# Optimization experiments

Measured on AMD Instinct MI355X. Metric: run time of the kernel, lower is better.

Reference implementation:

```python
import jax, jax.numpy as jnp
import numpy as np

N = 50000          # nodes
E = 800000         # edges (avg degree 16)
ROLE_DIM = 16
LAY_DIM = 16
G_IN = 96          # graph_in
H = 96             # hidden_channels (two layers of 96)
G_OUT = 96         # graph_out
HID = 256          # dense hidden_dim
NUM_ROLES = 120
MAX_LAYOUT = 1025


def _lin_params(k, out_d, in_d, bias=True):
    kw, kb = jax.random.split(k)
    s = 1.0 / np.sqrt(in_d)
    W = jax.random.uniform(kw, (out_d, in_d), jnp.float32, -s, s)
    if bias:
        b = jax.random.uniform(kb, (out_d,), jnp.float32, -s, s)
        return W, b
    return W


def setup_inputs() -> dict:
    key = jax.random.key(0)
    ks = jax.random.split(key, 16)
    x_layout = jax.random.randint(ks[0], (N, 4), 0, MAX_LAYOUT)
    x_role = jax.random.randint(ks[1], (N,), 0, NUM_ROLES)
    edge_index = jax.random.randint(ks[2], (2, E), 0, N)
    layout_emb = jax.random.normal(ks[3], (MAX_LAYOUT, LAY_DIM), jnp.float32)
    role_emb = jax.random.normal(ks[4], (NUM_ROLES, ROLE_DIM), jnp.float32)
    lin_W, lin_b = _lin_params(ks[5], G_IN, ROLE_DIM + 4 * LAY_DIM)
    c0_lW, c0_lb = _lin_params(ks[6], H, G_IN)
    c0_rW = _lin_params(ks[7], H, G_IN, bias=False)
    c1_lW, c1_lb = _lin_params(ks[8], H, H)
    c1_rW = _lin_params(ks[9], H, H, bias=False)
    c2_lW, c2_lb = _lin_params(ks[10], G_OUT, H)
    c2_rW = _lin_params(ks[11], G_OUT, H, bias=False)
    d0_W, d0_b = _lin_params(ks[12], HID, G_OUT)
    d1_W, d1_b = _lin_params(ks[13], HID, HID)
    d2_W, d2_b = _lin_params(ks[14], 1, HID)
    return dict(x_layout=x_layout, x_role=x_role, edge_index=edge_index,
                layout_emb=layout_emb, role_emb=role_emb,
                lin_W=lin_W, lin_b=lin_b,
                c0_lW=c0_lW, c0_lb=c0_lb, c0_rW=c0_rW,
                c1_lW=c1_lW, c1_lb=c1_lb, c1_rW=c1_rW,
                c2_lW=c2_lW, c2_lb=c2_lb, c2_rW=c2_rW,
                d0_W=d0_W, d0_b=d0_b, d1_W=d1_W, d1_b=d1_b,
                d2_W=d2_W, d2_b=d2_b)


def _sage(x, src, dst, lW, lb, rW):
    # SAGEConv (mean aggr): out = lin_l(mean_{j->i} x_j) + lin_r(x_i)
    msg = x[src]                                               # [E, D] gather
    ssum = jax.ops.segment_sum(msg, dst, num_segments=N)       # [N, D]
    cnt = jax.ops.segment_sum(jnp.ones((src.shape[0],), x.dtype), dst,
                              num_segments=N)                  # [N]
    agg = ssum / jnp.maximum(cnt, 1.0)[:, None]
    return agg @ lW.T + lb + x @ rW.T


def reference(x_layout, x_role, edge_index, layout_emb, role_emb,
              lin_W, lin_b,
              c0_lW, c0_lb, c0_rW,
              c1_lW, c1_lb, c1_rW,
              c2_lW, c2_lb, c2_rW,
              d0_W, d0_b, d1_W, d1_b, d2_W, d2_b):
    # embed + concat: [N, 4*16] layout embeds + [N, 16] role embed
    lay = layout_emb[x_layout].reshape(x_layout.shape[0], 4 * LAY_DIM)
    x = jnp.concatenate([lay, role_emb[x_role]], axis=1)       # [N, 80]
    x = x @ lin_W.T + lin_b                                    # [N, G_IN]
    # masked_select with x_role != -100: all indices valid here -> identity
    src, dst = edge_index[0], edge_index[1]
    x = jax.nn.relu(_sage(x, src, dst, c0_lW, c0_lb, c0_rW))
    x = jax.nn.relu(_sage(x, src, dst, c1_lW, c1_lb, c1_rW))
    x = jax.nn.relu(_sage(x, src, dst, c2_lW, c2_lb, c2_rW))
    # dense head (dropout p=0 -> identity)
    x = jax.nn.relu(x @ d0_W.T + d0_b)
    x = jax.nn.relu(x @ d1_W.T + d1_b)
    return x @ d2_W.T + d2_b                                   # [N, 1]
```

## Files before the change

kernel.cpp:

```cpp
#include <hip/hip_runtime.h>
#include <cstddef>


#define NB 256

using f16x4 = __attribute__((ext_vector_type(4))) _Float16;
using f32x4 = __attribute__((ext_vector_type(4))) float;

__global__ __launch_bounds__(NB) void count_int_kernel(const int* __restrict__ dst,
                                                       int* __restrict__ cnt, int E) {
    int e = blockIdx.x * NB + threadIdx.x;
    if (e < E) atomicAdd(&cnt[dst[e]], 1);
}

__global__ __launch_bounds__(NB) void scan_part1(const int* __restrict__ cnt,
                                                 int* __restrict__ part, int n) {
    __shared__ int ws[4];
    const int tid = threadIdx.x;
    const int base = blockIdx.x * 2048 + tid * 8;
    int s = 0;
#pragma unroll
    for (int q = 0; q < 8; ++q) {
        int i = base + q;
        if (i < n) s += cnt[i];
    }
#pragma unroll
    for (int off = 1; off < 64; off <<= 1) s += __shfl_xor(s, off);
    if ((tid & 63) == 0) ws[tid >> 6] = s;
    __syncthreads();
    if (tid == 0) part[blockIdx.x] = ws[0] + ws[1] + ws[2] + ws[3];
}

__global__ __launch_bounds__(64) void scan_part2(int* __restrict__ part,
                                                 int* __restrict__ rowptr,
                                                 int nb, int n) {
    const int lane = threadIdx.x;
    int v = (lane < nb) ? part[lane] : 0;
    int incl = v;
#pragma unroll
    for (int off = 1; off < 64; off <<= 1) {
        int u = __shfl_up(incl, off);
        if (lane >= off) incl += u;
    }
    if (lane < nb) part[lane] = incl - v;
    if (lane == 63) rowptr[n] = incl;
}

__global__ __launch_bounds__(NB) void scan_part3(const int* __restrict__ cnt,
                                                 const int* __restrict__ part,
                                                 int* __restrict__ rowptr,
                                                 int* __restrict__ cursor, int n) {
    __shared__ int ws[4];
    const int tid = threadIdx.x;
    const int lane = tid & 63, w = tid >> 6;
    const int base = blockIdx.x * 2048 + tid * 8;
    int loc[8];
    int s = 0;
#pragma unroll
    for (int q = 0; q < 8; ++q) {
        int i = base + q;
        int v = (i < n) ? cnt[i] : 0;
        loc[q] = s;
        s += v;
    }
    int incl = s;
#pragma unroll
    for (int off = 1; off < 64; off <<= 1) {
        int u = __shfl_up(incl, off);
        if (lane >= off) incl += u;
    }
    if (lane == 63) ws[w] = incl;
    __syncthreads();
    int woff = 0;
    for (int i = 0; i < w; ++i) woff += ws[i];
    int gbase = part[blockIdx.x] + woff + (incl - s);
#pragma unroll
    for (int q = 0; q < 8; ++q) {
        int i = base + q;
        if (i < n) {
            int v = gbase + loc[q];
            rowptr[i] = v;
            cursor[i] = v;
        }
    }
}

__global__ __launch_bounds__(NB) void fill_csr_kernel(const int* __restrict__ src,
                                                      const int* __restrict__ dst,
                                                      int* __restrict__ cursor,
                                                      int* __restrict__ col, int E) {
    int e = blockIdx.x * NB + threadIdx.x;
    if (e >= E) return;
    int p = atomicAdd(&cursor[dst[e]], 1);
    col[p] = src[e];
}

__global__ __launch_bounds__(NB) void gather_mean_kernel(
    const float* __restrict__ X, const int* __restrict__ rowptr,
    const int* __restrict__ col, float* __restrict__ G, int N) {
    int idx = blockIdx.x * NB + threadIdx.x;
    int node = idx / 24;
    if (node >= N) return;
    int c = idx - node * 24;
    const int s = rowptr[node], pe = rowptr[node + 1];
    float4 acc = {0.f, 0.f, 0.f, 0.f};
    int p = s;
    for (; p + 3 < pe; p += 4) {
        int j0 = col[p], j1 = col[p + 1], j2 = col[p + 2], j3 = col[p + 3];
        float4 v0 = *reinterpret_cast<const float4*>(&X[(size_t)j0 * 96 + 4 * c]);
        float4 v1 = *reinterpret_cast<const float4*>(&X[(size_t)j1 * 96 + 4 * c]);
        float4 v2 = *reinterpret_cast<const float4*>(&X[(size_t)j2 * 96 + 4 * c]);
        float4 v3 = *reinterpret_cast<const float4*>(&X[(size_t)j3 * 96 + 4 * c]);
        acc.x += (v0.x + v1.x) + (v2.x + v3.x);
        acc.y += (v0.y + v1.y) + (v2.y + v3.y);
        acc.z += (v0.z + v1.z) + (v2.z + v3.z);
        acc.w += (v0.w + v1.w) + (v2.w + v3.w);
    }
    for (; p < pe; ++p) {
        int j = col[p];
        float4 v = *reinterpret_cast<const float4*>(&X[(size_t)j * 96 + 4 * c]);
        acc.x += v.x; acc.y += v.y; acc.z += v.z; acc.w += v.w;
    }
    int deg = pe - s;
    float inv = (deg > 0) ? 1.f / (float)deg : 0.f;
    acc.x *= inv; acc.y *= inv; acc.z *= inv; acc.w *= inv;
    *reinterpret_cast<float4*>(&G[(size_t)node * 96 + 4 * c]) = acc;
}

__device__ inline void cvt_split(float4 f, f16x4& hi, f16x4& lo) {
    _Float16 h0 = (_Float16)f.x, h1 = (_Float16)f.y;
    _Float16 h2 = (_Float16)f.z, h3 = (_Float16)f.w;
    hi = (f16x4){h0, h1, h2, h3};
    lo = (f16x4){(_Float16)(f.x - (float)h0), (_Float16)(f.y - (float)h1),
                 (_Float16)(f.z - (float)h2), (_Float16)(f.w - (float)h3)};
}

template <int K, int OUT, int TC, int BK, bool RELU, bool SAGE, bool EMB, bool FDOT>
__global__ __launch_bounds__(NB) void gemm_mfma(
    const float* __restrict__ X, const float* __restrict__ G,
    const float* __restrict__ Wx, const float* __restrict__ Wg,
    const float* __restrict__ bias,
    const int* __restrict__ xl, const int* __restrict__ xr,
    const float* __restrict__ lemb, const float* __restrict__ remb,
    const float* __restrict__ d2w, const float* __restrict__ d2b,
    float* __restrict__ Y, int nrows) {
    constexpr int BM = 64;
    constexpr int BN = 2 * TC * 16;
    constexpr int CT = OUT / BN;
    constexpr int KT = SAGE ? 2 * K : K;
    constexpr int QX = BK / 4;
    constexpr int ST = BK + 4;
    constexpr int RX = (BM * QX + NB - 1) / NB;
    constexpr int RW = (BN * QX + NB - 1) / NB;
    __shared__ alignas(16) _Float16 Xhi[BM][ST];
    __shared__ alignas(16) _Float16 Xlo[BM][ST];
    __shared__ alignas(16) _Float16 Whi[BN][ST];
    __shared__ alignas(16) _Float16 Wlo[BN][ST];

    const int t = threadIdx.x;
    const int lane = t & 63;
    const int wave = t >> 6;
    const int lm = lane & 15, lg = lane >> 4;
    const int wm = (wave >> 1) * 32;
    const int wn = (wave & 1) * (TC * 16);

    const int bid = blockIdx.x;
    const int rowBase = (bid / CT) * BM;
    const int colTile = bid % CT;
    const int colBase = colTile * BN;

    float4 xreg[RX], wreg[RW];

    auto loadstep = [&](int k0) {
        const bool isG = SAGE && (k0 >= K);
        const float* __restrict__ Xp = isG ? G : X;
        const float* __restrict__ Wp = isG ? Wg : Wx;
        const int kl = isG ? (k0 - K) : k0;
#pragma unroll
        for (int rr = 0; rr < RX; ++rr) {
            int v = t + rr * NB;
            if (v < BM * QX) {
                int q = v % QX, m = v / QX;
                int r = rowBase + m;
                float4 f = {0.f, 0.f, 0.f, 0.f};
                if (r < nrows) {
                    if (EMB) {
                        int kk = kl + 4 * q;
                        if (kk < 64) {
                            int l = kk >> 4, c = kk & 15;
                            f = *reinterpret_cast<const float4*>(
                                &lemb[(size_t)xl[r * 4 + l] * 16 + c]);
                        } else {
                            f = *reinterpret_cast<const float4*>(
                                &remb[(size_t)xr[r] * 16 + (kk - 64)]);
                        }
                    } else {
                        f = *reinterpret_cast<const float4*>(
                            &Xp[(size_t)r * K + kl + 4 * q]);
                    }
                }
                xreg[rr] = f;
            }
        }
#pragma unroll
        for (int rr = 0; rr < RW; ++rr) {
            int v = t + rr * NB;
            if (v < BN * QX) {
                int q = v % QX, n = v / QX;
                wreg[rr] = *reinterpret_cast<const float4*>(
                    &Wp[(size_t)(colBase + n) * K + kl + 4 * q]);
            }
        }
    };

    auto storestep = [&]() {
#pragma unroll
        for (int rr = 0; rr < RX; ++rr) {
            int v = t + rr * NB;
            if (v < BM * QX) {
                int q = v % QX, m = v / QX;
                f16x4 hi, lo;
                cvt_split(xreg[rr], hi, lo);
                *reinterpret_cast<f16x4*>(&Xhi[m][4 * q]) = hi;
                *reinterpret_cast<f16x4*>(&Xlo[m][4 * q]) = lo;
            }
        }
#pragma unroll
        for (int rr = 0; rr < RW; ++rr) {
            int v = t + rr * NB;
            if (v < BN * QX) {
                int q = v % QX, n = v / QX;
                f16x4 hi, lo;
                cvt_split(wreg[rr], hi, lo);
                *reinterpret_cast<f16x4*>(&Whi[n][4 * q]) = hi;
                *reinterpret_cast<f16x4*>(&Wlo[n][4 * q]) = lo;
            }
        }
    };

    f32x4 acc[2][TC];
#pragma unroll
    for (int tr = 0; tr < 2; ++tr)
#pragma unroll
        for (int tc = 0; tc < TC; ++tc) acc[tr][tc] = (f32x4){0.f, 0.f, 0.f, 0.f};

    loadstep(0);
    for (int k0 = 0; k0 < KT; k0 += BK) {
        if (k0 > 0) __syncthreads();
        storestep();
        __syncthreads();
        if (k0 + BK < KT) loadstep(k0 + BK);

#pragma unroll
        for (int g = 0; g < BK / 16; ++g) {
            f16x4 ah[2], al[2], bh[TC], bl[TC];
#pragma unroll
            for (int tr = 0; tr < 2; ++tr) {
                ah[tr] = *reinterpret_cast<const f16x4*>(
                    &Xhi[wm + tr * 16 + lm][g * 16 + 4 * lg]);
                al[tr] = *reinterpret_cast<const f16x4*>(
                    &Xlo[wm + tr * 16 + lm][g * 16 + 4 * lg]);
            }
#pragma unroll
            for (int tc = 0; tc < TC; ++tc) {
                bh[tc] = *reinterpret_cast<const f16x4*>(
                    &Whi[wn + tc * 16 + lm][g * 16 + 4 * lg]);
                bl[tc] = *reinterpret_cast<const f16x4*>(
                    &Wlo[wn + tc * 16 + lm][g * 16 + 4 * lg]);
            }
#pragma unroll
            for (int tr = 0; tr < 2; ++tr)
#pragma unroll
                for (int tc = 0; tc < TC; ++tc) {
                    acc[tr][tc] = __builtin_amdgcn_mfma_f32_16x16x16f16(
                        ah[tr], bh[tc], acc[tr][tc], 0, 0, 0);
                    acc[tr][tc] = __builtin_amdgcn_mfma_f32_16x16x16f16(
                        ah[tr], bl[tc], acc[tr][tc], 0, 0, 0);
                    acc[tr][tc] = __builtin_amdgcn_mfma_f32_16x16x16f16(
                        al[tr], bh[tc], acc[tr][tc], 0, 0, 0);
                }
        }
    }

    if (!FDOT) {
#pragma unroll
        for (int tr = 0; tr < 2; ++tr)
#pragma unroll
            for (int tc = 0; tc < TC; ++tc) {
                int c = colBase + wn + tc * 16 + lm;
#pragma unroll
                for (int j = 0; j < 4; ++j) {
                    int r = rowBase + wm + tr * 16 + 4 * lg + j;
                    if (r >= nrows) continue;
                    float v = acc[tr][tc][j] + bias[c];
                    if (RELU) v = fmaxf(v, 0.f);
                    Y[(size_t)r * OUT + c] = v;
                }
            }
    } else {
#pragma unroll
        for (int tr = 0; tr < 2; ++tr) {
            float p[4] = {0.f, 0.f, 0.f, 0.f};
#pragma unroll
            for (int tc = 0; tc < TC; ++tc) {
                int c = colBase + wn + tc * 16 + lm;
                float bv = bias[c];
                float dw = d2w[c];
#pragma unroll
                for (int j = 0; j < 4; ++j) {
                    float v = fmaxf(acc[tr][tc][j] + bv, 0.f);
                    p[j] += v * dw;
                }
            }
#pragma unroll
            for (int j = 0; j < 4; ++j) {
                float s = p[j];
#pragma unroll
                for (int off = 1; off < 16; off <<= 1) s += __shfl_xor(s, off);
                int r = rowBase + wm + tr * 16 + 4 * lg + j;
                if (lm == 0 && r < nrows) {
                    float extra = (colTile == 0 && wn == 0) ? d2b[0] : 0.f;
                    atomicAdd(&Y[r], s + extra);
                }
            }
        }
    }
}

extern "C" void kernel_launch(void* const* d_in, const int* in_sizes, int n_in,
                              void* d_out, int out_size, void* d_ws, size_t ws_size,
                              hipStream_t stream) {
    const int*   x_layout = (const int*)d_in[0];
    const int*   x_role   = (const int*)d_in[1];
    const int*   ei       = (const int*)d_in[2];
    const float* lemb     = (const float*)d_in[3];
    const float* remb     = (const float*)d_in[4];
    const float* lin_W    = (const float*)d_in[5];
    const float* lin_b    = (const float*)d_in[6];
    const float* c0_lW    = (const float*)d_in[7];
    const float* c0_lb    = (const float*)d_in[8];
    const float* c0_rW    = (const float*)d_in[9];
    const float* c1_lW    = (const float*)d_in[10];
    const float* c1_lb    = (const float*)d_in[11];
    const float* c1_rW    = (const float*)d_in[12];
    const float* c2_lW    = (const float*)d_in[13];
    const float* c2_lb    = (const float*)d_in[14];
    const float* c2_rW    = (const float*)d_in[15];
    const float* d0_W     = (const float*)d_in[16];
    const float* d0_b     = (const float*)d_in[17];
    const float* d1_W     = (const float*)d_in[18];
    const float* d1_b     = (const float*)d_in[19];
    const float* d2_W     = (const float*)d_in[20];
    const float* d2_b     = (const float*)d_in[21];

    const int N = in_sizes[1];
    const int E = in_sizes[2] / 2;
    const int* src = ei;
    const int* dst = ei + E;

    float* ws     = (float*)d_ws;
    float* H0     = ws;
    int*   rowptr = (int*)d_ws;
    int*   cursor = rowptr + (N + 1);
    int*   col    = cursor + N;
    int*   part   = col + E;
    float* A      = ws + (size_t)256 * N;
    float* B      = A + (size_t)96 * N;
    float* C      = B + (size_t)96 * N;

    const dim3 blk(NB);
    const int rt64 = (N + 63) / 64;
    const int nbScan = (N + 2047) / 2048;
    const dim3 gE((E + NB - 1) / NB);
    const dim3 gGather(((size_t)N * 24 + NB - 1) / NB);

    hipMemsetAsync(cursor, 0, (size_t)N * sizeof(int), stream);
    count_int_kernel<<<gE, blk, 0, stream>>>(dst, cursor, E);
    scan_part1<<<dim3(nbScan), blk, 0, stream>>>(cursor, part, N);
    scan_part2<<<dim3(1), dim3(64), 0, stream>>>(part, rowptr, nbScan, N);
    scan_part3<<<dim3(nbScan), blk, 0, stream>>>(cursor, part, rowptr, cursor, N);
    fill_csr_kernel<<<gE, blk, 0, stream>>>(src, dst, cursor, col, E);

    gemm_mfma<80, 96, 3, 16, false, false, true, false>
        <<<dim3(rt64), blk, 0, stream>>>(
        nullptr, nullptr, lin_W, nullptr, lin_b,
        x_layout, x_role, lemb, remb, nullptr, nullptr, A, N);

    gather_mean_kernel<<<gGather, blk, 0, stream>>>(A, rowptr, col, B, N);
    gemm_mfma<96, 96, 3, 32, true, true, false, false>
        <<<dim3(rt64), blk, 0, stream>>>(
        A, B, c0_rW, c0_lW, c0_lb, nullptr, nullptr, nullptr, nullptr,
        nullptr, nullptr, C, N);

    gather_mean_kernel<<<gGather, blk, 0, stream>>>(C, rowptr, col, B, N);
    gemm_mfma<96, 96, 3, 32, true, true, false, false>
        <<<dim3(rt64), blk, 0, stream>>>(
        C, B, c1_rW, c1_lW, c1_lb, nullptr, nullptr, nullptr, nullptr,
        nullptr, nullptr, A, N);

    gather_mean_kernel<<<gGather, blk, 0, stream>>>(A, rowptr, col, B, N);
    gemm_mfma<96, 96, 3, 32, true, true, false, false>
        <<<dim3(rt64), blk, 0, stream>>>(
        A, B, c2_rW, c2_lW, c2_lb, nullptr, nullptr, nullptr, nullptr,
        nullptr, nullptr, C, N);

    gemm_mfma<96, 256, 4, 32, true, false, false, false>
        <<<dim3(rt64 * 2), blk, 0, stream>>>(
        C, nullptr, d0_W, nullptr, d0_b, nullptr, nullptr, nullptr, nullptr,
        nullptr, nullptr, H0, N);

    hipMemsetAsync(d_out, 0, (size_t)N * sizeof(float), stream);
    gemm_mfma<256, 256, 4, 32, true, false, false, true>
        <<<dim3(rt64 * 2), blk, 0, stream>>>(
        H0, nullptr, d1_W, nullptr, d1_b, nullptr, nullptr, nullptr, nullptr,
        d2_W, d2_b, (float*)d_out, N);
}
```

Before: 500.3 us.

## Fuse neighbor mean aggregation into SAGE layer GEMM kernel

Replaces the separate gather_mean kernel plus dual-input GEMM with a single sage_fused kernel per layer. Each 64-row block first gathers and averages its neighbors' features straight into shared memory as split fp16 hi/lo, then runs the MFMA GEMM over the self features and the aggregated features. This removes the global write and re-read of the aggregated matrix and one launch per layer. In exchange the gather becomes a serial prologue inside each GEMM block, shared memory use rises, and occupancy may drop.

```diff
diff --git a/kernel.cpp b/kernel.cpp
--- a/kernel.cpp
+++ b/kernel.cpp
@@ -95,38 +95,6 @@
     col[p] = src[e];
 }
 
-__global__ __launch_bounds__(NB) void gather_mean_kernel(
-    const float* __restrict__ X, const int* __restrict__ rowptr,
-    const int* __restrict__ col, float* __restrict__ G, int N) {
-    int idx = blockIdx.x * NB + threadIdx.x;
-    int node = idx / 24;
-    if (node >= N) return;
-    int c = idx - node * 24;
-    const int s = rowptr[node], pe = rowptr[node + 1];
-    float4 acc = {0.f, 0.f, 0.f, 0.f};
-    int p = s;
-    for (; p + 3 < pe; p += 4) {
-        int j0 = col[p], j1 = col[p + 1], j2 = col[p + 2], j3 = col[p + 3];
-        float4 v0 = *reinterpret_cast<const float4*>(&X[(size_t)j0 * 96 + 4 * c]);
-        float4 v1 = *reinterpret_cast<const float4*>(&X[(size_t)j1 * 96 + 4 * c]);
-        float4 v2 = *reinterpret_cast<const float4*>(&X[(size_t)j2 * 96 + 4 * c]);
-        float4 v3 = *reinterpret_cast<const float4*>(&X[(size_t)j3 * 96 + 4 * c]);
-        acc.x += (v0.x + v1.x) + (v2.x + v3.x);
-        acc.y += (v0.y + v1.y) + (v2.y + v3.y);
-        acc.z += (v0.z + v1.z) + (v2.z + v3.z);
-        acc.w += (v0.w + v1.w) + (v2.w + v3.w);
-    }
-    for (; p < pe; ++p) {
-        int j = col[p];
-        float4 v = *reinterpret_cast<const float4*>(&X[(size_t)j * 96 + 4 * c]);
-        acc.x += v.x; acc.y += v.y; acc.z += v.z; acc.w += v.w;
-    }
-    int deg = pe - s;
-    float inv = (deg > 0) ? 1.f / (float)deg : 0.f;
-    acc.x *= inv; acc.y *= inv; acc.z *= inv; acc.w *= inv;
-    *reinterpret_cast<float4*>(&G[(size_t)node * 96 + 4 * c]) = acc;
-}
-
 __device__ inline void cvt_split(float4 f, f16x4& hi, f16x4& lo) {
     _Float16 h0 = (_Float16)f.x, h1 = (_Float16)f.y;
     _Float16 h2 = (_Float16)f.z, h3 = (_Float16)f.w;
@@ -135,11 +103,184 @@
                  (_Float16)(f.z - (float)h2), (_Float16)(f.w - (float)h3)};
 }
 
-template <int K, int OUT, int TC, int BK, bool RELU, bool SAGE, bool EMB, bool FDOT>
+__global__ __launch_bounds__(NB) void sage_fused(
+    const float* __restrict__ X, const int* __restrict__ rowptr,
+    const int* __restrict__ col,
+    const float* __restrict__ Wx, const float* __restrict__ Wg,
+    const float* __restrict__ bias, float* __restrict__ Y, int nrows) {
+    constexpr int BM = 64, BN = 96, BK = 32, TC = 3;
+    constexpr int QX = BK / 4;
+    constexpr int ST = BK + 4;
+    constexpr int GS = 100;
+    constexpr int RX = BM * QX / NB;
+    constexpr int RW = BN * QX / NB;
+    __shared__ alignas(16) _Float16 Ghi[BM][GS];
+    __shared__ alignas(16) _Float16 Glo[BM][GS];
+    __shared__ alignas(16) _Float16 Xhi[BM][ST];
+    __shared__ alignas(16) _Float16 Xlo[BM][ST];
+    __shared__ alignas(16) _Float16 Whi[BN][ST];
+    __shared__ alignas(16) _Float16 Wlo[BN][ST];
+
+    const int t = threadIdx.x;
+    const int lane = t & 63;
+    const int wave = t >> 6;
+    const int lm = lane & 15, lg = lane >> 4;
+    const int wm = (wave >> 1) * 32;
+    const int wn = (wave & 1) * (TC * 16);
+    const int rowBase = blockIdx.x * BM;
+
+    for (int slot = t; slot < BM * 24; slot += NB) {
+        int ml = slot / 24, c = slot - ml * 24;
+        int r = rowBase + ml;
+        float4 acc = {0.f, 0.f, 0.f, 0.f};
+        if (r < nrows) {
+            const int s = rowptr[r], pe = rowptr[r + 1];
+            int p = s;
+            for (; p + 3 < pe; p += 4) {
+                int j0 = col[p], j1 = col[p + 1], j2 = col[p + 2], j3 = col[p + 3];
+                float4 v0 = *reinterpret_cast<const float4*>(&X[(size_t)j0 * 96 + 4 * c]);
+                float4 v1 = *reinterpret_cast<const float4*>(&X[(size_t)j1 * 96 + 4 * c]);
+                float4 v2 = *reinterpret_cast<const float4*>(&X[(size_t)j2 * 96 + 4 * c]);
+                float4 v3 = *reinterpret_cast<const float4*>(&X[(size_t)j3 * 96 + 4 * c]);
+                acc.x += (v0.x + v1.x) + (v2.x + v3.x);
+                acc.y += (v0.y + v1.y) + (v2.y + v3.y);
+                acc.z += (v0.z + v1.z) + (v2.z + v3.z);
+                acc.w += (v0.w + v1.w) + (v2.w + v3.w);
+            }
+            for (; p < pe; ++p) {
+                int j = col[p];
+                float4 v = *reinterpret_cast<const float4*>(&X[(size_t)j * 96 + 4 * c]);
+                acc.x += v.x; acc.y += v.y; acc.z += v.z; acc.w += v.w;
+            }
+            int deg = pe - s;
+            float inv = (deg > 0) ? 1.f / (float)deg : 0.f;
+            acc.x *= inv; acc.y *= inv; acc.z *= inv; acc.w *= inv;
+        }
+        f16x4 hi, lo;
+        cvt_split(acc, hi, lo);
+        *reinterpret_cast<f16x4*>(&Ghi[ml][4 * c]) = hi;
+        *reinterpret_cast<f16x4*>(&Glo[ml][4 * c]) = lo;
+    }
+
+    float4 xreg[RX], wreg[RW];
+
+    auto loadstep = [&](int step) {
+        const bool isX = (step < 3);
+        const int kl = isX ? step * BK : (step - 3) * BK;
+        if (isX) {
+#pragma unroll
+            for (int rr = 0; rr < RX; ++rr) {
+                int v = t + rr * NB;
+                int q = v % QX, m = v / QX;
+                int r = rowBase + m;
+                float4 f = {0.f, 0.f, 0.f, 0.f};
+                if (r < nrows)
+                    f = *reinterpret_cast<const float4*>(&X[(size_t)r * 96 + kl + 4 * q]);
+                xreg[rr] = f;
+            }
+        }
+        const float* __restrict__ Wp = isX ? Wx : Wg;
+#pragma unroll
+        for (int rr = 0; rr < RW; ++rr) {
+            int v = t + rr * NB;
+            int q = v % QX, n = v / QX;
+            wreg[rr] = *reinterpret_cast<const float4*>(
+                &Wp[(size_t)n * 96 + kl + 4 * q]);
+        }
+    };
+
+    auto storestep = [&](bool isX) {
+        if (isX) {
+#pragma unroll
+            for (int rr = 0; rr < RX; ++rr) {
+                int v = t + rr * NB;
+                int q = v % QX, m = v / QX;
+                f16x4 hi, lo;
+                cvt_split(xreg[rr], hi, lo);
+                *reinterpret_cast<f16x4*>(&Xhi[m][4 * q]) = hi;
+                *reinterpret_cast<f16x4*>(&Xlo[m][4 * q]) = lo;
+            }
+        }
+#pragma unroll
+        for (int rr = 0; rr < RW; ++rr) {
+            int v = t + rr * NB;
+            int q = v % QX, n = v / QX;
+            f16x4 hi, lo;
+            cvt_split(wreg[rr], hi, lo);
+            *reinterpret_cast<f16x4*>(&Whi[n][4 * q]) = hi;
+            *reinterpret_cast<f16x4*>(&Wlo[n][4 * q]) = lo;
+        }
+    };
+
+    f32x4 acc[2][TC];
+#pragma unroll
+    for (int tr = 0; tr < 2; ++tr)
+#pragma unroll
+        for (int tc = 0; tc < TC; ++tc) acc[tr][tc] = (f32x4){0.f, 0.f, 0.f, 0.f};
+
+    loadstep(0);
+    for (int step = 0; step < 6; ++step) {
+        const bool isX = (step < 3);
+        __syncthreads();
+        storestep(isX);
+        __syncthreads();
+        if (step + 1 < 6) loadstep(step + 1);
+
+        const int gofs = isX ? 0 : (step - 3) * BK;
+#pragma unroll
+        for (int g = 0; g < BK / 16; ++g) {
+            f16x4 ah[2], al[2], bh[TC], bl[TC];
+#pragma unroll
+            for (int tr = 0; tr < 2; ++tr) {
+                int row = wm + tr * 16 + lm;
+                if (isX) {
+                    ah[tr] = *reinterpret_cast<const f16x4*>(&Xhi[row][g * 16 + 4 * lg]);
+                    al[tr] = *reinterpret_cast<const f16x4*>(&Xlo[row][g * 16 + 4 * lg]);
+                } else {
+                    ah[tr] = *reinterpret_cast<const f16x4*>(&Ghi[row][gofs + g * 16 + 4 * lg]);
+                    al[tr] = *reinterpret_cast<const f16x4*>(&Glo[row][gofs + g * 16 + 4 * lg]);
+                }
+            }
+#pragma unroll
+            for (int tc = 0; tc < TC; ++tc) {
+                bh[tc] = *reinterpret_cast<const f16x4*>(
+                    &Whi[wn + tc * 16 + lm][g * 16 + 4 * lg]);
+                bl[tc] = *reinterpret_cast<const f16x4*>(
+                    &Wlo[wn + tc * 16 + lm][g * 16 + 4 * lg]);
+            }
+#pragma unroll
+            for (int tr = 0; tr < 2; ++tr)
+#pragma unroll
+                for (int tc = 0; tc < TC; ++tc) {
+                    acc[tr][tc] = __builtin_amdgcn_mfma_f32_16x16x16f16(
+                        ah[tr], bh[tc], acc[tr][tc], 0, 0, 0);
+                    acc[tr][tc] = __builtin_amdgcn_mfma_f32_16x16x16f16(
+                        ah[tr], bl[tc], acc[tr][tc], 0, 0, 0);
+                    acc[tr][tc] = __builtin_amdgcn_mfma_f32_16x16x16f16(
+                        al[tr], bh[tc], acc[tr][tc], 0, 0, 0);
+                }
+        }
+    }
+
+#pragma unroll
+    for (int tr = 0; tr < 2; ++tr)
+#pragma unroll
+        for (int tc = 0; tc < TC; ++tc) {
+            int c = wn + tc * 16 + lm;
+#pragma unroll
+            for (int j = 0; j < 4; ++j) {
+                int r = rowBase + wm + tr * 16 + 4 * lg + j;
+                if (r >= nrows) continue;
+                float v = acc[tr][tc][j] + bias[c];
+                Y[(size_t)r * 96 + c] = fmaxf(v, 0.f);
+            }
+        }
+}
+
+template <int K, int OUT, int TC, int BK, bool RELU, bool EMB, bool FDOT>
 __global__ __launch_bounds__(NB) void gemm_mfma(
-    const float* __restrict__ X, const float* __restrict__ G,
-    const float* __restrict__ Wx, const float* __restrict__ Wg,
-    const float* __restrict__ bias,
+    const float* __restrict__ X,
+    const float* __restrict__ Wx, const float* __restrict__ bias,
     const int* __restrict__ xl, const int* __restrict__ xr,
     const float* __restrict__ lemb, const float* __restrict__ remb,
     const float* __restrict__ d2w, const float* __restrict__ d2b,
@@ -147,7 +288,6 @@
     constexpr int BM = 64;
     constexpr int BN = 2 * TC * 16;
     constexpr int CT = OUT / BN;
-    constexpr int KT = SAGE ? 2 * K : K;
     constexpr int QX = BK / 4;
     constexpr int ST = BK + 4;
     constexpr int RX = (BM * QX + NB - 1) / NB;
@@ -171,11 +311,7 @@
 
     float4 xreg[RX], wreg[RW];
 
-    auto loadstep = [&](int k0) {
-        const bool isG = SAGE && (k0 >= K);
-        const float* __restrict__ Xp = isG ? G : X;
-        const float* __restrict__ Wp = isG ? Wg : Wx;
-        const int kl = isG ? (k0 - K) : k0;
+    auto loadstep = [&](int kl) {
 #pragma unroll
         for (int rr = 0; rr < RX; ++rr) {
             int v = t + rr * NB;
@@ -196,7 +332,7 @@
                         }
                     } else {
                         f = *reinterpret_cast<const float4*>(
-                            &Xp[(size_t)r * K + kl + 4 * q]);
+                            &X[(size_t)r * K + kl + 4 * q]);
                     }
                 }
                 xreg[rr] = f;
@@ -208,7 +344,7 @@
             if (v < BN * QX) {
                 int q = v % QX, n = v / QX;
                 wreg[rr] = *reinterpret_cast<const float4*>(
-                    &Wp[(size_t)(colBase + n) * K + kl + 4 * q]);
+                    &Wx[(size_t)(colBase + n) * K + kl + 4 * q]);
             }
         }
     };
@@ -245,11 +381,11 @@
         for (int tc = 0; tc < TC; ++tc) acc[tr][tc] = (f32x4){0.f, 0.f, 0.f, 0.f};
 
     loadstep(0);
-    for (int k0 = 0; k0 < KT; k0 += BK) {
+    for (int k0 = 0; k0 < K; k0 += BK) {
         if (k0 > 0) __syncthreads();
         storestep();
         __syncthreads();
-        if (k0 + BK < KT) loadstep(k0 + BK);
+        if (k0 + BK < K) loadstep(k0 + BK);
 
 #pragma unroll
         for (int g = 0; g < BK / 16; ++g) {
@@ -365,14 +501,12 @@
     int*   col    = cursor + N;
     int*   part   = col + E;
     float* A      = ws + (size_t)256 * N;
-    float* B      = A + (size_t)96 * N;
-    float* C      = B + (size_t)96 * N;
+    float* C      = A + (size_t)96 * N;
 
     const dim3 blk(NB);
     const int rt64 = (N + 63) / 64;
     const int nbScan = (N + 2047) / 2048;
     const dim3 gE((E + NB - 1) / NB);
-    const dim3 gGather(((size_t)N * 24 + NB - 1) / NB);
 
     hipMemsetAsync(cursor, 0, (size_t)N * sizeof(int), stream);
     count_int_kernel<<<gE, blk, 0, stream>>>(dst, cursor, E);
@@ -381,37 +515,26 @@
     scan_part3<<<dim3(nbScan), blk, 0, stream>>>(cursor, part, rowptr, cursor, N);
     fill_csr_kernel<<<gE, blk, 0, stream>>>(src, dst, cursor, col, E);
 
-    gemm_mfma<80, 96, 3, 16, false, false, true, false>
+    gemm_mfma<80, 96, 3, 16, false, true, false>
         <<<dim3(rt64), blk, 0, stream>>>(
-        nullptr, nullptr, lin_W, nullptr, lin_b,
-        x_layout, x_role, lemb, remb, nullptr, nullptr, A, N);
-
-    gather_mean_kernel<<<gGather, blk, 0, stream>>>(A, rowptr, col, B, N);
-    gemm_mfma<96, 96, 3, 32, true, true, false, false>
-        <<<dim3(rt64), blk, 0, stream>>>(
-        A, B, c0_rW, c0_lW, c0_lb, nullptr, nullptr, nullptr, nullptr,
-        nullptr, nullptr, C, N);
-
-    gather_mean_kernel<<<gGather, blk, 0, stream>>>(C, rowptr, col, B, N);
-    gemm_mfma<96, 96, 3, 32, true, true, false, false>
-        <<<dim3(rt64), blk, 0, stream>>>(
-        C, B, c1_rW, c1_lW, c1_lb, nullptr, nullptr, nullptr, nullptr,
+        nullptr, lin_W, lin_b, x_layout, x_role, lemb, remb,
         nullptr, nullptr, A, N);
 
-    gather_mean_kernel<<<gGather, blk, 0, stream>>>(A, rowptr, col, B, N);
-    gemm_mfma<96, 96, 3, 32, true, true, false, false>
-        <<<dim3(rt64), blk, 0, stream>>>(
-        A, B, c2_rW, c2_lW, c2_lb, nullptr, nullptr, nullptr, nullptr,
-        nullptr, nullptr, C, N);
-
-    gemm_mfma<96, 256, 4, 32, true, false, false, false>
+    sage_fused<<<dim3(rt64), blk, 0, stream>>>(
+        A, rowptr, col, c0_rW, c0_lW, c0_lb, C, N);
+    sage_fused<<<dim3(rt64), blk, 0, stream>>>(
+        C, rowptr, col, c1_rW, c1_lW, c1_lb, A, N);
+    sage_fused<<<dim3(rt64), blk, 0, stream>>>(
+        A, rowptr, col, c2_rW, c2_lW, c2_lb, C, N);
+
+    gemm_mfma<96, 256, 4, 32, true, false, false>
         <<<dim3(rt64 * 2), blk, 0, stream>>>(
-        C, nullptr, d0_W, nullptr, d0_b, nullptr, nullptr, nullptr, nullptr,
+        C, d0_W, d0_b, nullptr, nullptr, nullptr, nullptr,
         nullptr, nullptr, H0, N);
 
     hipMemsetAsync(d_out, 0, (size_t)N * sizeof(float), stream);
-    gemm_mfma<256, 256, 4, 32, true, false, false, true>
+    gemm_mfma<256, 256, 4, 32, true, false, true>
         <<<dim3(rt64 * 2), blk, 0, stream>>>(
-        H0, nullptr, d1_W, nullptr, d1_b, nullptr, nullptr, nullptr, nullptr,
+        H0, d1_W, d1_b, nullptr, nullptr, nullptr, nullptr,
         d2_W, d2_b, (float*)d_out, N);
 }
```

After: 543.7 us. +8.7%, slower.
